# Optimization experiments

Hardware: AMD Instinct MI355X
Metric: run time of the kernel (lower is better)

## Reference

```python
import jax, jax.numpy as jnp
import numpy as np

N_NODES = 20000
N_EDGES = 200000
D_IN = 32      # nf_input_dim
D_H = 32       # nf_hide_dim
D_OUT = 8      # nf_output_dim
E_DIM = 16     # edge_dim


def setup_inputs() -> dict:
    key = jax.random.key(0)
    ks = jax.random.split(key, 20)
    s = 0.1
    inp = {
        "x": jax.random.normal(ks[0], (N_NODES, D_IN), jnp.float32),
        "edge_attr": jax.random.normal(ks[1], (N_EDGES, E_DIM), jnp.float32),
        "edge_index": jax.random.randint(ks[2], (2, N_EDGES), 0, N_NODES, jnp.int32),
    }
    # layer 0: edge MLP (E_DIM->E_DIM->D_IN*D_H), root [D_IN,D_H], bias [D_H]
    inp["w1_0"] = jax.random.normal(ks[3], (E_DIM, E_DIM), jnp.float32) * s
    inp["b1_0"] = jnp.zeros((E_DIM,), jnp.float32)
    inp["w2_0"] = jax.random.normal(ks[4], (E_DIM, D_IN * D_H), jnp.float32) * s
    inp["b2_0"] = jnp.zeros((D_IN * D_H,), jnp.float32)
    inp["root_0"] = jax.random.normal(ks[5], (D_IN, D_H), jnp.float32) * s
    inp["bias_0"] = jnp.zeros((D_H,), jnp.float32)
    # layer 1: edge MLP (E_DIM->E_DIM->D_H*D_H), root [D_H,D_H], bias [D_H]
    inp["w1_1"] = jax.random.normal(ks[6], (E_DIM, E_DIM), jnp.float32) * s
    inp["b1_1"] = jnp.zeros((E_DIM,), jnp.float32)
    inp["w2_1"] = jax.random.normal(ks[7], (E_DIM, D_H * D_H), jnp.float32) * s
    inp["b2_1"] = jnp.zeros((D_H * D_H,), jnp.float32)
    inp["root_1"] = jax.random.normal(ks[8], (D_H, D_H), jnp.float32) * s
    inp["bias_1"] = jnp.zeros((D_H,), jnp.float32)
    # classifier
    inp["cls_w"] = jax.random.normal(ks[9], (D_H, D_OUT), jnp.float32) * s
    inp["cls_b"] = jnp.zeros((D_OUT,), jnp.float32)
    return inp


def _nnconv(x, edge_attr, src, dst, inv_count, w1, b1, w2, b2, root, bias, din, dout, n):
    # edge network: Linear -> ELU -> Linear producing per-edge weight matrix [E, din, dout]
    h = jax.nn.elu(edge_attr @ w1 + b1)
    theta = (h @ w2 + b2).reshape(-1, din, dout)
    # gather source features, per-edge matvec, scatter-mean into dst
    msg = jnp.einsum("ei,eio->eo", x[src], theta)          # [E, dout]
    agg = jax.ops.segment_sum(msg, dst, num_segments=n) * inv_count[:, None]
    return agg + x @ root + bias                            # root weight + bias (PyG defaults)


def reference(x, edge_attr, edge_index,
              w1_0, b1_0, w2_0, b2_0, root_0, bias_0,
              w1_1, b1_1, w2_1, b2_1, root_1, bias_1,
              cls_w, cls_b):
    n = x.shape[0]
    src, dst = edge_index[0], edge_index[1]
    deg = jax.ops.segment_sum(jnp.ones(src.shape[0], x.dtype), dst, num_segments=n)
    inv_count = 1.0 / jnp.maximum(deg, 1.0)
    h = jax.nn.elu(_nnconv(x, edge_attr, src, dst, inv_count,
                           w1_0, b1_0, w2_0, b2_0, root_0, bias_0, D_IN, D_H, n))
    h = jax.nn.elu(_nnconv(h, edge_attr, src, dst, inv_count,
                           w1_1, b1_1, w2_1, b2_1, root_1, bias_1, D_H, D_H, n))
    # dropout is identity in eval mode
    return h @ cls_w + cls_b
```

## Files before the change

### kernel.cpp

```cpp
#include <hip/hip_runtime.h>
#include <hip/hip_bf16.h>
#include <math.h>

#define N_NODES 20000
#define N_EDGES 200000
#define D_H 32
#define E_DIM 16
#define CAP 40
#define NTILES (N_EDGES / 16)
#define NJOBS (NTILES / 2)
#define W2S_SHORTS (17 * 2 * 64 * 8)
#define PREP_SHORTS (W2S_SHORTS + 512)

typedef __attribute__((ext_vector_type(8))) short bf16x8;
typedef __attribute__((ext_vector_type(4))) float f32x4;

__device__ __forceinline__ float elu_f(float v) { return v > 0.f ? v : expm1f(v); }
__device__ __forceinline__ short f2bf(float f) {
    union { __hip_bfloat16 h; short s; } u;
    u.h = __float2bfloat16(f);
    return u.s;
}
__device__ __forceinline__ float bf2f(__hip_bfloat16 h) { return __bfloat162float(h); }

__global__ __launch_bounds__(256)
void init_kernel(const float* __restrict__ w2_0, const float* __restrict__ b2_0,
                 const float* __restrict__ w1_0, const float* __restrict__ b1_0,
                 const float* __restrict__ w2_1, const float* __restrict__ b2_1,
                 const float* __restrict__ w1_1, const float* __restrict__ b1_1,
                 int* __restrict__ cnt, short* __restrict__ prep)
{
    const int gid = blockIdx.x * 256 + threadIdx.x;
    if (gid < N_NODES) cnt[gid] = 0;
    if (gid < 2 * PREP_SHORTS) {
        int layer = gid >= PREP_SHORTS ? 1 : 0;
        int r = gid - layer * PREP_SHORTS;
        const float* w2 = layer ? w2_1 : w2_0;
        const float* b2 = layer ? b2_1 : b2_0;
        const float* w1 = layer ? w1_1 : w1_0;
        const float* b1 = layer ? b1_1 : b1_0;
        float v;
        if (r < W2S_SHORTS) {
            int j = r & 7, l = (r >> 3) & 63, ct = (r >> 9) & 1, kk = r >> 10;
            int ii = (l >> 4) * 8 + j;
            int o = ct * 16 + (l & 15);
            v = (kk < 16) ? w2[kk * 1024 + ii * 32 + o] : b2[ii * 32 + o];
        } else {
            int q = r - W2S_SHORTS;
            int j = q & 7, l = q >> 3;
            int m = l & 15, k = (l >> 4) * 8 + j;
            v = (k < 16) ? w1[k * 16 + m] : (k == 16 ? b1[m] : 0.f);
        }
        prep[gid] = f2bf(v);
    }
}

__global__ __launch_bounds__(256)
void hist_kernel(const int* __restrict__ dst, int* __restrict__ cnt, int* __restrict__ ord) {
    int e = blockIdx.x * 256 + threadIdx.x;
    if (e < N_EDGES) ord[e] = atomicAdd(&cnt[dst[e]], 1);
}

__global__ __launch_bounds__(1024)
void scan_kernel(const int* __restrict__ cnt, int* __restrict__ rowptr) {
    __shared__ int part[1024];
    const int t = threadIdx.x;
    const int base = t * 20;
    int loc[20];
    int sum = 0;
    #pragma unroll
    for (int j = 0; j < 20; ++j) {
        int idx = base + j;
        int v = (idx < N_NODES) ? cnt[idx] : 0;
        loc[j] = v;
        sum += v;
    }
    part[t] = sum;
    __syncthreads();
    for (int off = 1; off < 1024; off <<= 1) {
        int v = (t >= off) ? part[t - off] : 0;
        __syncthreads();
        part[t] += v;
        __syncthreads();
    }
    int run = part[t] - sum;
    #pragma unroll
    for (int j = 0; j < 20; ++j) {
        int idx = base + j;
        if (idx < N_NODES) { rowptr[idx] = run; run += loc[j]; }
    }
    if (t == 0) rowptr[N_NODES] = N_EDGES;
}

template<int MODE, bool BF16IN>
__global__ __launch_bounds__(512)
void edge_kernel(const void* __restrict__ xin_,
                 const float* __restrict__ edge_attr,
                 const int* __restrict__ src,
                 const int* __restrict__ dst,
                 int* __restrict__ cnt,
                 int* __restrict__ pebuf,
                 const int* __restrict__ ord,
                 const int* __restrict__ rowptr,
                 const short* __restrict__ prepL,
                 __hip_bfloat16* __restrict__ msg)
{
    __shared__ __align__(16) short w2s[PREP_SHORTS];

    const int t = threadIdx.x;
    for (int i = t; i < PREP_SHORTS / 8; i += 512)
        ((int4*)w2s)[i] = ((const int4*)prepL)[i];
    __syncthreads();

    const int lane = t & 63;
    const int wave = t >> 6;
    const int job = blockIdx.x * 8 + wave;
    if (job >= NJOBS) return;
    const int eloc = lane & 15;
    const int kg = lane >> 4;

    const int e0 = job * 32 + eloc;
    const int e1 = e0 + 16;

    int pe0, pe1;
    if (MODE == 0) {
        int p0_ = 0, p1_ = 0;
        if (kg == 0) {
            const int d0 = dst[e0], d1 = dst[e1];
            p0_ = d0 * CAP + atomicAdd(&cnt[d0], 1);
            p1_ = d1 * CAP + atomicAdd(&cnt[d1], 1);
            pebuf[e0] = p0_;
            pebuf[e1] = p1_;
        }
        pe0 = __shfl(p0_, eloc);
        pe1 = __shfl(p1_, eloc);
    } else if (MODE == 1) {
        pe0 = pebuf[e0];
        pe1 = pebuf[e1];
    } else {
        pe0 = rowptr[dst[e0]] + ord[e0];
        pe1 = rowptr[dst[e1]] + ord[e1];
    }

    const int sn0 = src[e0], sn1 = src[e1];

    bf16x8 xf0, xf1;
    if (BF16IN) {
        const short* xb = (const short*)xin_;
        xf0 = *(const bf16x8*)(xb + (size_t)sn0 * 32 + kg * 8);
        xf1 = *(const bf16x8*)(xb + (size_t)sn1 * 32 + kg * 8);
    } else {
        const float* xf = (const float*)xin_;
        const float4 xa0 = *(const float4*)(xf + (size_t)sn0 * 32 + kg * 8);
        const float4 xa1 = *(const float4*)(xf + (size_t)sn0 * 32 + kg * 8 + 4);
        const float4 xb0 = *(const float4*)(xf + (size_t)sn1 * 32 + kg * 8);
        const float4 xb1 = *(const float4*)(xf + (size_t)sn1 * 32 + kg * 8 + 4);
        xf0[0]=f2bf(xa0.x); xf0[1]=f2bf(xa0.y); xf0[2]=f2bf(xa0.z); xf0[3]=f2bf(xa0.w);
        xf0[4]=f2bf(xa1.x); xf0[5]=f2bf(xa1.y); xf0[6]=f2bf(xa1.z); xf0[7]=f2bf(xa1.w);
        xf1[0]=f2bf(xb0.x); xf1[1]=f2bf(xb0.y); xf1[2]=f2bf(xb0.z); xf1[3]=f2bf(xb0.w);
        xf1[4]=f2bf(xb1.x); xf1[5]=f2bf(xb1.y); xf1[6]=f2bf(xb1.z); xf1[7]=f2bf(xb1.w);
    }

    bf16x8 ea0 = {0,0,0,0,0,0,0,0}, ea1 = {0,0,0,0,0,0,0,0};
    if (kg < 2) {
        const float4 p0 = *(const float4*)(edge_attr + (size_t)e0 * E_DIM + kg * 8);
        const float4 p1 = *(const float4*)(edge_attr + (size_t)e0 * E_DIM + kg * 8 + 4);
        ea0[0]=f2bf(p0.x); ea0[1]=f2bf(p0.y); ea0[2]=f2bf(p0.z); ea0[3]=f2bf(p0.w);
        ea0[4]=f2bf(p1.x); ea0[5]=f2bf(p1.y); ea0[6]=f2bf(p1.z); ea0[7]=f2bf(p1.w);
        const float4 q0 = *(const float4*)(edge_attr + (size_t)e1 * E_DIM + kg * 8);
        const float4 q1 = *(const float4*)(edge_attr + (size_t)e1 * E_DIM + kg * 8 + 4);
        ea1[0]=f2bf(q0.x); ea1[1]=f2bf(q0.y); ea1[2]=f2bf(q0.z); ea1[3]=f2bf(q0.w);
        ea1[4]=f2bf(q1.x); ea1[5]=f2bf(q1.y); ea1[6]=f2bf(q1.z); ea1[7]=f2bf(q1.w);
    } else if (kg == 2) {
        ea0[0] = f2bf(1.0f);
        ea1[0] = f2bf(1.0f);
    }

    const f32x4 zero4 = {0.f, 0.f, 0.f, 0.f};

    bf16x8 w1f = *(const bf16x8*)&w2s[W2S_SHORTS + lane * 8];
    f32x4 hd0 = __builtin_amdgcn_mfma_f32_16x16x32_bf16(w1f, ea0, zero4, 0, 0, 0);
    f32x4 hd1 = __builtin_amdgcn_mfma_f32_16x16x32_bf16(w1f, ea1, zero4, 0, 0, 0);
    float hv0[4], hv1[4];
    #pragma unroll
    for (int r = 0; r < 4; ++r) { hv0[r] = elu_f(hd0[r]); hv1[r] = elu_f(hd1[r]); }

    float m00[4]={0,0,0,0}, m01[4]={0,0,0,0}, m10[4]={0,0,0,0}, m11[4]={0,0,0,0};
    #pragma unroll
    for (int kk = 0; kk < 17; ++kk) {
        bf16x8 a0 = *(const bf16x8*)&w2s[(kk * 2 + 0) * 512 + lane * 8];
        bf16x8 a1 = *(const bf16x8*)&w2s[(kk * 2 + 1) * 512 + lane * 8];
        float h0, h1;
        if (kk < 16) {
            h0 = __shfl(hv0[kk & 3], (kk >> 2) * 16 + eloc);
            h1 = __shfl(hv1[kk & 3], (kk >> 2) * 16 + eloc);
        } else {
            h0 = 1.0f; h1 = 1.0f;
        }
        f32x4 d00 = __builtin_amdgcn_mfma_f32_16x16x32_bf16(a0, xf0, zero4, 0, 0, 0);
        f32x4 d01 = __builtin_amdgcn_mfma_f32_16x16x32_bf16(a1, xf0, zero4, 0, 0, 0);
        f32x4 d10 = __builtin_amdgcn_mfma_f32_16x16x32_bf16(a0, xf1, zero4, 0, 0, 0);
        f32x4 d11 = __builtin_amdgcn_mfma_f32_16x16x32_bf16(a1, xf1, zero4, 0, 0, 0);
        #pragma unroll
        for (int r = 0; r < 4; ++r) {
            m00[r] += h0 * d00[r]; m01[r] += h0 * d01[r];
            m10[r] += h1 * d10[r]; m11[r] += h1 * d11[r];
        }
    }

    short* mp0 = (short*)(msg + (size_t)pe0 * D_H);
    short* mp1 = (short*)(msg + (size_t)pe1 * D_H);
    short q00[4] = { f2bf(m00[0]), f2bf(m00[1]), f2bf(m00[2]), f2bf(m00[3]) };
    short q01[4] = { f2bf(m01[0]), f2bf(m01[1]), f2bf(m01[2]), f2bf(m01[3]) };
    short q10[4] = { f2bf(m10[0]), f2bf(m10[1]), f2bf(m10[2]), f2bf(m10[3]) };
    short q11[4] = { f2bf(m11[0]), f2bf(m11[1]), f2bf(m11[2]), f2bf(m11[3]) };
    *(int2*)(mp0 + kg * 4)      = *(int2*)q00;
    *(int2*)(mp0 + 16 + kg * 4) = *(int2*)q01;
    *(int2*)(mp1 + kg * 4)      = *(int2*)q10;
    *(int2*)(mp1 + 16 + kg * 4) = *(int2*)q11;
}

template<bool LAST, bool PADDED>
__global__ __launch_bounds__(256)
void agg_kernel(const void* __restrict__ xin_,
                const __hip_bfloat16* __restrict__ msg,
                const int* __restrict__ rowptr,
                const int* __restrict__ cnt,
                const float* __restrict__ root,
                const float* __restrict__ bias,
                const float* __restrict__ cls_w,
                const float* __restrict__ cls_b,
                __hip_bfloat16* __restrict__ hout,
                float* __restrict__ out)
{
    __shared__ float root_s[32 * 32];
    __shared__ float bias_s[32];
    __shared__ float h2_s[4][33];
    const int t = threadIdx.x;
    for (int i = t; i < 1024; i += 256) root_s[i] = root[i];
    if (t < 32) bias_s[t] = bias[t];
    __syncthreads();

    const int lane = t & 63;
    const int wave = t >> 6;
    const int o = lane & 31;
    const int half = lane >> 5;
    const int n = blockIdx.x * 4 + wave;

    int start, end;
    if (PADDED) { start = n * CAP; end = start + cnt[n]; }
    else        { start = rowptr[n]; end = rowptr[n + 1]; }

    float s = 0.f;
    int j = start + half;
    for (; j + 6 < end; j += 8) {
        float v0 = bf2f(msg[(size_t)(j    ) * D_H + o]);
        float v1 = bf2f(msg[(size_t)(j + 2) * D_H + o]);
        float v2 = bf2f(msg[(size_t)(j + 4) * D_H + o]);
        float v3 = bf2f(msg[(size_t)(j + 6) * D_H + o]);
        s += (v0 + v1) + (v2 + v3);
    }
    for (; j < end; j += 2)
        s += bf2f(msg[(size_t)j * D_H + o]);
    s += __shfl_xor(s, 32);

    float acc = s * (1.f / fmaxf((float)(end - start), 1.f)) + bias_s[o];
    const float xv = LAST ? bf2f(((const __hip_bfloat16*)xin_)[(size_t)n * 32 + o])
                          : ((const float*)xin_)[(size_t)n * 32 + o];
    #pragma unroll
    for (int i = 0; i < 32; ++i)
        acc += __shfl(xv, half * 32 + i) * root_s[i * 32 + o];
    acc = elu_f(acc);

    if (!LAST) {
        if (half == 0) hout[(size_t)n * 32 + o] = __float2bfloat16(acc);
    } else {
        if (half == 0) h2_s[wave][o] = acc;
        __syncthreads();
        if (t < 32) {
            const int nn = t >> 3, jj = t & 7;
            float a = cls_b[jj];
            #pragma unroll
            for (int i = 0; i < 32; ++i) a += h2_s[nn][i] * cls_w[i * 8 + jj];
            out[(size_t)(blockIdx.x * 4 + nn) * 8 + jj] = a;
        }
    }
}

extern "C" void kernel_launch(void* const* d_in, const int* in_sizes, int n_in,
                              void* d_out, int out_size, void* d_ws, size_t ws_size,
                              hipStream_t stream)
{
    const float* x          = (const float*)d_in[0];
    const float* edge_attr  = (const float*)d_in[1];
    const int*   edge_index = (const int*)d_in[2];
    const float* w1_0 = (const float*)d_in[3];
    const float* b1_0 = (const float*)d_in[4];
    const float* w2_0 = (const float*)d_in[5];
    const float* b2_0 = (const float*)d_in[6];
    const float* root_0 = (const float*)d_in[7];
    const float* bias_0 = (const float*)d_in[8];
    const float* w1_1 = (const float*)d_in[9];
    const float* b1_1 = (const float*)d_in[10];
    const float* w2_1 = (const float*)d_in[11];
    const float* b2_1 = (const float*)d_in[12];
    const float* root_1 = (const float*)d_in[13];
    const float* bias_1 = (const float*)d_in[14];
    const float* cls_w = (const float*)d_in[15];
    const float* cls_b = (const float*)d_in[16];

    const int* src = edge_index;
    const int* dst = edge_index + N_EDGES;

    const int EB = (N_EDGES + 255) / 256;
    const int IB = (2 * PREP_SHORTS + 255) / 256;
    const int GB = (NJOBS + 7) / 8;

    size_t need = 0;
    size_t o_cnt = need;  need += (size_t)N_NODES * 4;
    size_t o_pe  = need;  need += (size_t)N_EDGES * 4;
    size_t o_prep= (need + 15) & ~(size_t)15; need = o_prep + (size_t)2 * PREP_SHORTS * 2;
    size_t o_msg = (need + 63) & ~(size_t)63; need = o_msg + (size_t)N_NODES * CAP * D_H * 2;
    size_t o_hb  = (need + 15) & ~(size_t)15; need = o_hb + (size_t)N_NODES * D_H * 2;

    char* ws = (char*)d_ws;

    if (ws_size >= need) {
        int* cnt = (int*)(ws + o_cnt);
        int* pe  = (int*)(ws + o_pe);
        short* prep = (short*)(ws + o_prep);
        __hip_bfloat16* msg  = (__hip_bfloat16*)(ws + o_msg);
        __hip_bfloat16* hbuf = (__hip_bfloat16*)(ws + o_hb);

        init_kernel<<<IB, 256, 0, stream>>>(w2_0, b2_0, w1_0, b1_0,
                                            w2_1, b2_1, w1_1, b1_1, cnt, prep);
        edge_kernel<0, false><<<GB, 512, 0, stream>>>(x, edge_attr, src, dst,
                                                      cnt, pe, nullptr, nullptr, prep, msg);
        agg_kernel<false, true><<<N_NODES / 4, 256, 0, stream>>>(x, msg, nullptr, cnt,
                                                                 root_0, bias_0, nullptr, nullptr,
                                                                 hbuf, nullptr);
        edge_kernel<1, true><<<GB, 512, 0, stream>>>(hbuf, edge_attr, src, dst,
                                                     nullptr, pe, nullptr, nullptr,
                                                     prep + PREP_SHORTS, msg);
        agg_kernel<true, true><<<N_NODES / 4, 256, 0, stream>>>(hbuf, msg, nullptr, cnt,
                                                                root_1, bias_1, cls_w, cls_b,
                                                                nullptr, (float*)d_out);
    } else {
        int* cnt    = (int*)ws;
        int* rowptr = cnt + N_NODES;
        int* ord    = rowptr + N_NODES + 1;
        size_t off = ((size_t)(2 * N_NODES + 1 + N_EDGES) * 4 + 15) & ~(size_t)15;
        short* prep = (short*)(ws + off);
        off = (off + (size_t)2 * PREP_SHORTS * 2 + 15) & ~(size_t)15;
        __hip_bfloat16* msg = (__hip_bfloat16*)(ws + off);
        off = (off + (size_t)N_EDGES * D_H * 2 + 15) & ~(size_t)15;
        __hip_bfloat16* hbuf = (__hip_bfloat16*)(ws + off);

        init_kernel<<<IB, 256, 0, stream>>>(w2_0, b2_0, w1_0, b1_0,
                                            w2_1, b2_1, w1_1, b1_1, cnt, prep);
        hist_kernel<<<EB, 256, 0, stream>>>(dst, cnt, ord);
        scan_kernel<<<1, 1024, 0, stream>>>(cnt, rowptr);

        edge_kernel<2, false><<<GB, 512, 0, stream>>>(x, edge_attr, src, dst,
                                                      nullptr, nullptr, ord, rowptr, prep, msg);
        agg_kernel<false, false><<<N_NODES / 4, 256, 0, stream>>>(x, msg, rowptr, nullptr,
                                                                  root_0, bias_0, nullptr, nullptr,
                                                                  hbuf, nullptr);
        edge_kernel<2, true><<<GB, 512, 0, stream>>>(hbuf, edge_attr, src, dst,
                                                     nullptr, nullptr, ord, rowptr,
                                                     prep + PREP_SHORTS, msg);
        agg_kernel<true, false><<<N_NODES / 4, 256, 0, stream>>>(hbuf, msg, rowptr, nullptr,
                                                                 root_1, bias_1, cls_w, cls_b,
                                                                 nullptr, (float*)d_out);
    }
}
```

Baseline: 94.18 us.

## Process four edge tiles per wave and vectorize bf16 message aggregation

The edge kernel now handles 64 edges per wave instead of 32. Each weight fragment read from LDS feeds eight MFMAs instead of four, which doubles reuse of the shared weight tile and halves the number of waves. The aggregation kernel now reads two bf16 channels per 32-bit load, with four row groups per wave and a two-step shuffle reduction, and each lane produces two output channels. The cost is higher register pressure in the edge kernel, which may lower occupancy, and fewer waves available to hide gather latency.

Result: slower. 107.5 us (+14.1%).

```diff
diff --git a/kernel.cpp b/kernel.cpp
--- a/kernel.cpp
+++ b/kernel.cpp
@@ -7,8 +7,7 @@
 #define D_H 32
 #define E_DIM 16
 #define CAP 40
-#define NTILES (N_EDGES / 16)
-#define NJOBS (NTILES / 2)
+#define NSLOTS (N_EDGES / 64)
 #define W2S_SHORTS (17 * 2 * 64 * 8)
 #define PREP_SHORTS (W2S_SHORTS + 512)
 
@@ -114,66 +113,75 @@
 
     const int lane = t & 63;
     const int wave = t >> 6;
-    const int job = blockIdx.x * 8 + wave;
-    if (job >= NJOBS) return;
+    const int slot = blockIdx.x * 8 + wave;
+    if (slot >= NSLOTS) return;
     const int eloc = lane & 15;
     const int kg = lane >> 4;
 
-    const int e0 = job * 32 + eloc;
+    const int e0 = slot * 64 + eloc;
     const int e1 = e0 + 16;
-
-    int pe0, pe1;
+    const int e2 = e0 + 32;
+    const int e3 = e0 + 48;
+
+    int pe0, pe1, pe2, pe3;
     if (MODE == 0) {
-        int p0_ = 0, p1_ = 0;
+        int p0_ = 0, p1_ = 0, p2_ = 0, p3_ = 0;
         if (kg == 0) {
-            const int d0 = dst[e0], d1 = dst[e1];
+            const int d0 = dst[e0], d1 = dst[e1], d2 = dst[e2], d3 = dst[e3];
             p0_ = d0 * CAP + atomicAdd(&cnt[d0], 1);
             p1_ = d1 * CAP + atomicAdd(&cnt[d1], 1);
-            pebuf[e0] = p0_;
-            pebuf[e1] = p1_;
-        }
-        pe0 = __shfl(p0_, eloc);
-        pe1 = __shfl(p1_, eloc);
+            p2_ = d2 * CAP + atomicAdd(&cnt[d2], 1);
+            p3_ = d3 * CAP + atomicAdd(&cnt[d3], 1);
+            pebuf[e0] = p0_; pebuf[e1] = p1_;
+            pebuf[e2] = p2_; pebuf[e3] = p3_;
+        }
+        pe0 = __shfl(p0_, eloc); pe1 = __shfl(p1_, eloc);
+        pe2 = __shfl(p2_, eloc); pe3 = __shfl(p3_, eloc);
     } else if (MODE == 1) {
-        pe0 = pebuf[e0];
-        pe1 = pebuf[e1];
+        pe0 = pebuf[e0]; pe1 = pebuf[e1]; pe2 = pebuf[e2]; pe3 = pebuf[e3];
     } else {
         pe0 = rowptr[dst[e0]] + ord[e0];
         pe1 = rowptr[dst[e1]] + ord[e1];
-    }
-
-    const int sn0 = src[e0], sn1 = src[e1];
-
-    bf16x8 xf0, xf1;
+        pe2 = rowptr[dst[e2]] + ord[e2];
+        pe3 = rowptr[dst[e3]] + ord[e3];
+    }
+
+    const int sn0 = src[e0], sn1 = src[e1], sn2 = src[e2], sn3 = src[e3];
+
+    bf16x8 xf0, xf1, xf2, xf3;
     if (BF16IN) {
         const short* xb = (const short*)xin_;
         xf0 = *(const bf16x8*)(xb + (size_t)sn0 * 32 + kg * 8);
         xf1 = *(const bf16x8*)(xb + (size_t)sn1 * 32 + kg * 8);
+        xf2 = *(const bf16x8*)(xb + (size_t)sn2 * 32 + kg * 8);
+        xf3 = *(const bf16x8*)(xb + (size_t)sn3 * 32 + kg * 8);
     } else {
         const float* xf = (const float*)xin_;
-        const float4 xa0 = *(const float4*)(xf + (size_t)sn0 * 32 + kg * 8);
-        const float4 xa1 = *(const float4*)(xf + (size_t)sn0 * 32 + kg * 8 + 4);
-        const float4 xb0 = *(const float4*)(xf + (size_t)sn1 * 32 + kg * 8);
-        const float4 xb1 = *(const float4*)(xf + (size_t)sn1 * 32 + kg * 8 + 4);
-        xf0[0]=f2bf(xa0.x); xf0[1]=f2bf(xa0.y); xf0[2]=f2bf(xa0.z); xf0[3]=f2bf(xa0.w);
-        xf0[4]=f2bf(xa1.x); xf0[5]=f2bf(xa1.y); xf0[6]=f2bf(xa1.z); xf0[7]=f2bf(xa1.w);
-        xf1[0]=f2bf(xb0.x); xf1[1]=f2bf(xb0.y); xf1[2]=f2bf(xb0.z); xf1[3]=f2bf(xb0.w);
-        xf1[4]=f2bf(xb1.x); xf1[5]=f2bf(xb1.y); xf1[6]=f2bf(xb1.z); xf1[7]=f2bf(xb1.w);
-    }
-
-    bf16x8 ea0 = {0,0,0,0,0,0,0,0}, ea1 = {0,0,0,0,0,0,0,0};
+        #define LOADX(dstv, sn)                                                   \
+        {                                                                         \
+            const float4 a_ = *(const float4*)(xf + (size_t)(sn) * 32 + kg * 8);  \
+            const float4 b_ = *(const float4*)(xf + (size_t)(sn) * 32 + kg * 8 + 4);\
+            dstv[0]=f2bf(a_.x); dstv[1]=f2bf(a_.y); dstv[2]=f2bf(a_.z); dstv[3]=f2bf(a_.w);\
+            dstv[4]=f2bf(b_.x); dstv[5]=f2bf(b_.y); dstv[6]=f2bf(b_.z); dstv[7]=f2bf(b_.w);\
+        }
+        LOADX(xf0, sn0) LOADX(xf1, sn1) LOADX(xf2, sn2) LOADX(xf3, sn3)
+        #undef LOADX
+    }
+
+    bf16x8 ea0 = {0,0,0,0,0,0,0,0}, ea1 = ea0, ea2 = ea0, ea3 = ea0;
     if (kg < 2) {
-        const float4 p0 = *(const float4*)(edge_attr + (size_t)e0 * E_DIM + kg * 8);
-        const float4 p1 = *(const float4*)(edge_attr + (size_t)e0 * E_DIM + kg * 8 + 4);
-        ea0[0]=f2bf(p0.x); ea0[1]=f2bf(p0.y); ea0[2]=f2bf(p0.z); ea0[3]=f2bf(p0.w);
-        ea0[4]=f2bf(p1.x); ea0[5]=f2bf(p1.y); ea0[6]=f2bf(p1.z); ea0[7]=f2bf(p1.w);
-        const float4 q0 = *(const float4*)(edge_attr + (size_t)e1 * E_DIM + kg * 8);
-        const float4 q1 = *(const float4*)(edge_attr + (size_t)e1 * E_DIM + kg * 8 + 4);
-        ea1[0]=f2bf(q0.x); ea1[1]=f2bf(q0.y); ea1[2]=f2bf(q0.z); ea1[3]=f2bf(q0.w);
-        ea1[4]=f2bf(q1.x); ea1[5]=f2bf(q1.y); ea1[6]=f2bf(q1.z); ea1[7]=f2bf(q1.w);
+        #define LOADE(dstv, e)                                                            \
+        {                                                                                 \
+            const float4 a_ = *(const float4*)(edge_attr + (size_t)(e) * E_DIM + kg * 8); \
+            const float4 b_ = *(const float4*)(edge_attr + (size_t)(e) * E_DIM + kg * 8 + 4);\
+            dstv[0]=f2bf(a_.x); dstv[1]=f2bf(a_.y); dstv[2]=f2bf(a_.z); dstv[3]=f2bf(a_.w);\
+            dstv[4]=f2bf(b_.x); dstv[5]=f2bf(b_.y); dstv[6]=f2bf(b_.z); dstv[7]=f2bf(b_.w);\
+        }
+        LOADE(ea0, e0) LOADE(ea1, e1) LOADE(ea2, e2) LOADE(ea3, e3)
+        #undef LOADE
     } else if (kg == 2) {
-        ea0[0] = f2bf(1.0f);
-        ea1[0] = f2bf(1.0f);
+        ea0[0] = f2bf(1.0f); ea1[0] = f2bf(1.0f);
+        ea2[0] = f2bf(1.0f); ea3[0] = f2bf(1.0f);
     }
 
     const f32x4 zero4 = {0.f, 0.f, 0.f, 0.f};
@@ -181,43 +189,60 @@
     bf16x8 w1f = *(const bf16x8*)&w2s[W2S_SHORTS + lane * 8];
     f32x4 hd0 = __builtin_amdgcn_mfma_f32_16x16x32_bf16(w1f, ea0, zero4, 0, 0, 0);
     f32x4 hd1 = __builtin_amdgcn_mfma_f32_16x16x32_bf16(w1f, ea1, zero4, 0, 0, 0);
-    float hv0[4], hv1[4];
+    f32x4 hd2 = __builtin_amdgcn_mfma_f32_16x16x32_bf16(w1f, ea2, zero4, 0, 0, 0);
+    f32x4 hd3 = __builtin_amdgcn_mfma_f32_16x16x32_bf16(w1f, ea3, zero4, 0, 0, 0);
+    float hv0[4], hv1[4], hv2[4], hv3[4];
     #pragma unroll
-    for (int r = 0; r < 4; ++r) { hv0[r] = elu_f(hd0[r]); hv1[r] = elu_f(hd1[r]); }
+    for (int r = 0; r < 4; ++r) {
+        hv0[r] = elu_f(hd0[r]); hv1[r] = elu_f(hd1[r]);
+        hv2[r] = elu_f(hd2[r]); hv3[r] = elu_f(hd3[r]);
+    }
 
     float m00[4]={0,0,0,0}, m01[4]={0,0,0,0}, m10[4]={0,0,0,0}, m11[4]={0,0,0,0};
+    float m20[4]={0,0,0,0}, m21[4]={0,0,0,0}, m30[4]={0,0,0,0}, m31[4]={0,0,0,0};
     #pragma unroll
     for (int kk = 0; kk < 17; ++kk) {
         bf16x8 a0 = *(const bf16x8*)&w2s[(kk * 2 + 0) * 512 + lane * 8];
         bf16x8 a1 = *(const bf16x8*)&w2s[(kk * 2 + 1) * 512 + lane * 8];
-        float h0, h1;
+        float h0, h1, h2, h3;
         if (kk < 16) {
             h0 = __shfl(hv0[kk & 3], (kk >> 2) * 16 + eloc);
             h1 = __shfl(hv1[kk & 3], (kk >> 2) * 16 + eloc);
+            h2 = __shfl(hv2[kk & 3], (kk >> 2) * 16 + eloc);
+            h3 = __shfl(hv3[kk & 3], (kk >> 2) * 16 + eloc);
         } else {
-            h0 = 1.0f; h1 = 1.0f;
+            h0 = h1 = h2 = h3 = 1.0f;
         }
         f32x4 d00 = __builtin_amdgcn_mfma_f32_16x16x32_bf16(a0, xf0, zero4, 0, 0, 0);
         f32x4 d01 = __builtin_amdgcn_mfma_f32_16x16x32_bf16(a1, xf0, zero4, 0, 0, 0);
         f32x4 d10 = __builtin_amdgcn_mfma_f32_16x16x32_bf16(a0, xf1, zero4, 0, 0, 0);
         f32x4 d11 = __builtin_amdgcn_mfma_f32_16x16x32_bf16(a1, xf1, zero4, 0, 0, 0);
+        f32x4 d20 = __builtin_amdgcn_mfma_f32_16x16x32_bf16(a0, xf2, zero4, 0, 0, 0);
+        f32x4 d21 = __builtin_amdgcn_mfma_f32_16x16x32_bf16(a1, xf2, zero4, 0, 0, 0);
+        f32x4 d30 = __builtin_amdgcn_mfma_f32_16x16x32_bf16(a0, xf3, zero4, 0, 0, 0);
+        f32x4 d31 = __builtin_amdgcn_mfma_f32_16x16x32_bf16(a1, xf3, zero4, 0, 0, 0);
         #pragma unroll
         for (int r = 0; r < 4; ++r) {
             m00[r] += h0 * d00[r]; m01[r] += h0 * d01[r];
             m10[r] += h1 * d10[r]; m11[r] += h1 * d11[r];
-        }
-    }
-
-    short* mp0 = (short*)(msg + (size_t)pe0 * D_H);
-    short* mp1 = (short*)(msg + (size_t)pe1 * D_H);
-    short q00[4] = { f2bf(m00[0]), f2bf(m00[1]), f2bf(m00[2]), f2bf(m00[3]) };
-    short q01[4] = { f2bf(m01[0]), f2bf(m01[1]), f2bf(m01[2]), f2bf(m01[3]) };
-    short q10[4] = { f2bf(m10[0]), f2bf(m10[1]), f2bf(m10[2]), f2bf(m10[3]) };
-    short q11[4] = { f2bf(m11[0]), f2bf(m11[1]), f2bf(m11[2]), f2bf(m11[3]) };
-    *(int2*)(mp0 + kg * 4)      = *(int2*)q00;
-    *(int2*)(mp0 + 16 + kg * 4) = *(int2*)q01;
-    *(int2*)(mp1 + kg * 4)      = *(int2*)q10;
-    *(int2*)(mp1 + 16 + kg * 4) = *(int2*)q11;
+            m20[r] += h2 * d20[r]; m21[r] += h2 * d21[r];
+            m30[r] += h3 * d30[r]; m31[r] += h3 * d31[r];
+        }
+    }
+
+    #define STORE(pe, mA, mB)                                                 \
+    {                                                                         \
+        short* mp = (short*)(msg + (size_t)(pe) * D_H);                       \
+        short qa[4] = { f2bf(mA[0]), f2bf(mA[1]), f2bf(mA[2]), f2bf(mA[3]) }; \
+        short qb[4] = { f2bf(mB[0]), f2bf(mB[1]), f2bf(mB[2]), f2bf(mB[3]) }; \
+        *(int2*)(mp + kg * 4)      = *(int2*)qa;                              \
+        *(int2*)(mp + 16 + kg * 4) = *(int2*)qb;                              \
+    }
+    STORE(pe0, m00, m01)
+    STORE(pe1, m10, m11)
+    STORE(pe2, m20, m21)
+    STORE(pe3, m30, m31)
+    #undef STORE
 }
 
 template<bool LAST, bool PADDED>
@@ -243,39 +268,55 @@
 
     const int lane = t & 63;
     const int wave = t >> 6;
-    const int o = lane & 31;
-    const int half = lane >> 5;
+    const int c2 = lane & 15;
+    const int rg = lane >> 4;
     const int n = blockIdx.x * 4 + wave;
 
     int start, end;
     if (PADDED) { start = n * CAP; end = start + cnt[n]; }
     else        { start = rowptr[n]; end = rowptr[n + 1]; }
 
-    float s = 0.f;
-    int j = start + half;
-    for (; j + 6 < end; j += 8) {
-        float v0 = bf2f(msg[(size_t)(j    ) * D_H + o]);
-        float v1 = bf2f(msg[(size_t)(j + 2) * D_H + o]);
-        float v2 = bf2f(msg[(size_t)(j + 4) * D_H + o]);
-        float v3 = bf2f(msg[(size_t)(j + 6) * D_H + o]);
-        s += (v0 + v1) + (v2 + v3);
-    }
-    for (; j < end; j += 2)
-        s += bf2f(msg[(size_t)j * D_H + o]);
-    s += __shfl_xor(s, 32);
-
-    float acc = s * (1.f / fmaxf((float)(end - start), 1.f)) + bias_s[o];
-    const float xv = LAST ? bf2f(((const __hip_bfloat16*)xin_)[(size_t)n * 32 + o])
-                          : ((const float*)xin_)[(size_t)n * 32 + o];
+    const short* msp = (const short*)msg;
+    float s0 = 0.f, s1 = 0.f;
+    int j = start + rg;
+    for (; j + 4 < end; j += 8) {
+        unsigned va = *(const unsigned*)(msp + (size_t)j * D_H + c2 * 2);
+        unsigned vb = *(const unsigned*)(msp + (size_t)(j + 4) * D_H + c2 * 2);
+        s0 += __uint_as_float(va << 16) + __uint_as_float(vb << 16);
+        s1 += __uint_as_float(va & 0xffff0000u) + __uint_as_float(vb & 0xffff0000u);
+    }
+    for (; j < end; j += 4) {
+        unsigned va = *(const unsigned*)(msp + (size_t)j * D_H + c2 * 2);
+        s0 += __uint_as_float(va << 16);
+        s1 += __uint_as_float(va & 0xffff0000u);
+    }
+    s0 += __shfl_xor(s0, 16); s0 += __shfl_xor(s0, 32);
+    s1 += __shfl_xor(s1, 16); s1 += __shfl_xor(s1, 32);
+
+    const int o0 = c2 * 2, o1 = o0 + 1;
+    const float inv = 1.f / fmaxf((float)(end - start), 1.f);
+    float a0 = s0 * inv + bias_s[o0];
+    float a1 = s1 * inv + bias_s[o1];
+
+    const float xv = LAST ? bf2f(((const __hip_bfloat16*)xin_)[(size_t)n * 32 + (lane & 31)])
+                          : ((const float*)xin_)[(size_t)n * 32 + (lane & 31)];
     #pragma unroll
-    for (int i = 0; i < 32; ++i)
-        acc += __shfl(xv, half * 32 + i) * root_s[i * 32 + o];
-    acc = elu_f(acc);
+    for (int i = 0; i < 32; ++i) {
+        const float xi = __shfl(xv, i);
+        a0 += xi * root_s[i * 32 + o0];
+        a1 += xi * root_s[i * 32 + o1];
+    }
+    a0 = elu_f(a0);
+    a1 = elu_f(a1);
 
     if (!LAST) {
-        if (half == 0) hout[(size_t)n * 32 + o] = __float2bfloat16(acc);
+        if (rg == 0) {
+            unsigned pk = (unsigned)(unsigned short)f2bf(a0)
+                        | ((unsigned)(unsigned short)f2bf(a1) << 16);
+            *(unsigned*)((short*)hout + (size_t)n * 32 + o0) = pk;
+        }
     } else {
-        if (half == 0) h2_s[wave][o] = acc;
+        if (rg == 0) { h2_s[wave][o0] = a0; h2_s[wave][o1] = a1; }
         __syncthreads();
         if (t < 32) {
             const int nn = t >> 3, jj = t & 7;
@@ -314,7 +355,7 @@
 
     const int EB = (N_EDGES + 255) / 256;
     const int IB = (2 * PREP_SHORTS + 255) / 256;
-    const int GB = (NJOBS + 7) / 8;
+    const int GB = (NSLOTS + 7) / 8;
 
     size_t need = 0;
     size_t o_cnt = need;  need += (size_t)N_NODES * 4;
```
